# Optimization experiments

Measured on AMD Instinct MI355X. Metric: run time of the kernel, lower is better.

The kernel has to match this reference:

```python
import jax, jax.numpy as jnp
import numpy as np

INSTANCE_LOSS_WEIGHT = 5.0


def setup_inputs() -> dict:
    key = jax.random.key(0)
    k1, k2 = jax.random.split(key)
    B, NP, NT, H, W = 8, 8, 16, 512, 512
    pred_masks = jax.random.normal(k1, (B, NP, H, W), dtype=jnp.float32)   # logits
    target_masks = jax.random.uniform(k2, (B, NT, H, W), dtype=jnp.float32)  # targets in [0,1]
    return {"pred_masks": pred_masks, "target_masks": target_masks}


def reference(pred_masks, target_masks):
    # Multi-instance branch of SAMLossMultiInstance.forward (pred_masks.shape[1] > 1).
    # Original: per (i,j) pair, mean BCE-with-logits over pixels; pairs where
    # target j is all-zero are skipped (loss_matrix entry stays 0). Then
    # min over targets, mean over preds, mean over batch, * instance_loss_weight.
    #
    # Closed form: BCE(x, t) = softplus(x) - x*t, so
    #   mean_pix BCE(x_i, t_j) = mean(softplus(x_i)) - (x_i . t_j) / HW
    B, NP, H, W = pred_masks.shape
    HW = H * W
    s = jnp.mean(jax.nn.softplus(pred_masks), axis=(-2, -1))               # [B, NP]
    dots = jnp.einsum('bihw,bjhw->bij', pred_masks, target_masks) / HW     # [B, NP, NT]
    loss_matrix = s[:, :, None] - dots                                     # [B, NP, NT]
    # Empty targets are skipped in the original loop -> entry stays 0.
    t_empty = jnp.sum(target_masks, axis=(-2, -1)) == 0                    # [B, NT]
    loss_matrix = jnp.where(t_empty[:, None, :], 0.0, loss_matrix)
    min_losses = jnp.min(loss_matrix, axis=-1)                             # [B, NP]
    instance_loss = jnp.mean(min_losses)
    total_loss = INSTANCE_LOSS_WEIGHT * instance_loss
    return total_loss
```

## Files before the change

### kernel.cpp

```cpp
#include <hip/hip_runtime.h>

#define NB 8
#define NP 8
#define NT 16
#define HW (512 * 512)
#define HW4 (HW / 4)
#define NACC (NP + NP * NT + NT)
#define THREADS 256
#define BLOCKS_PER_B 256
#define NROW 32
#define LDSPITCH 153

__device__ __forceinline__ float softplus1(float x) {
  return fmaxf(x, 0.0f) + __logf(1.0f + __expf(-fabsf(x)));
}

__global__ __launch_bounds__(THREADS, 4) void sam_partial(
    const float* __restrict__ pred, const float* __restrict__ targ,
    float* __restrict__ ws) {
  const int b   = blockIdx.x >> 8;
  const int blk = blockIdx.x & 255;
  const int tid = threadIdx.x;
  const int idx = (blk << 8) | tid;
  const int lane = tid & 63;
  const int wid  = tid >> 6;
  const int row  = (wid << 3) | (lane >> 3);
  const bool wr  = (lane & 7) == 0;

  __shared__ float red[NROW][LDSPITCH];

  const float4* __restrict__ pb =
      reinterpret_cast<const float4*>(pred) + (size_t)b * NP * HW4;
  const float4* __restrict__ tb =
      reinterpret_cast<const float4*>(targ) + (size_t)b * NT * HW4;

  float4 p[NP];
#pragma unroll
  for (int i = 0; i < NP; ++i) p[i] = pb[(size_t)i * HW4 + idx];
  float4 t[NT];
#pragma unroll
  for (int j = 0; j < NT; ++j) t[j] = tb[(size_t)j * HW4 + idx];

#define STASH(a, expr)                                   \
  {                                                      \
    float v_ = (expr);                                   \
    v_ += __shfl_down(v_, 4);                            \
    v_ += __shfl_down(v_, 2);                            \
    v_ += __shfl_down(v_, 1);                            \
    if (wr) red[row][(a)] = v_;                          \
  }

#pragma unroll
  for (int i = 0; i < NP; ++i) {
    STASH(i, (softplus1(p[i].x) + softplus1(p[i].y)) +
             (softplus1(p[i].z) + softplus1(p[i].w)));
  }
#pragma unroll
  for (int i = 0; i < NP; ++i) {
#pragma unroll
    for (int j = 0; j < NT; ++j) {
      STASH(NP + i * NT + j,
            fmaf(p[i].x, t[j].x,
            fmaf(p[i].y, t[j].y,
            fmaf(p[i].z, t[j].z, p[i].w * t[j].w))));
    }
  }
#pragma unroll
  for (int j = 0; j < NT; ++j) {
    STASH(NP + NP * NT + j, (t[j].x + t[j].y) + (t[j].z + t[j].w));
  }
#undef STASH

  __syncthreads();
  if (tid < NACC) {
    float v = 0.0f;
#pragma unroll
    for (int r = 0; r < NROW; ++r) v += red[r][tid];
    atomicAdd(ws + (size_t)b * NACC + tid, v);
  }
}

__global__ void sam_final(const float* __restrict__ ws,
                          float* __restrict__ out) {
  const int t = threadIdx.x;
  const int b = t >> 3;
  const int i = t & 7;
  const float* w = ws + (size_t)b * NACC;
  const float spsum = w[i];
  float m = 3.4e38f;
#pragma unroll
  for (int j = 0; j < NT; ++j) {
    const float tsj = w[NP + NP * NT + j];
    const float v =
        (tsj == 0.0f) ? 0.0f : (spsum - w[NP + i * NT + j]) * (1.0f / HW);
    m = fminf(m, v);
  }
  float s = m;
#pragma unroll
  for (int off = 32; off > 0; off >>= 1) s += __shfl_down(s, off);
  if (t == 0) out[0] = 5.0f * s * (1.0f / 64.0f);
}

extern "C" void kernel_launch(void* const* d_in, const int* in_sizes, int n_in,
                              void* d_out, int out_size, void* d_ws,
                              size_t ws_size, hipStream_t stream) {
  const float* pred = (const float*)d_in[0];
  const float* targ = (const float*)d_in[1];
  float* out = (float*)d_out;
  float* ws = (float*)d_ws;

  hipMemsetAsync(ws, 0, (size_t)NB * NACC * sizeof(float), stream);
  sam_partial<<<dim3(NB * BLOCKS_PER_B), THREADS, 0, stream>>>(pred, targ, ws);
  sam_final<<<1, 64, 0, stream>>>(ws, out);
}
```

Baseline: 87.36 us.

## Split targets across waves and accumulate per-thread over pixel loop

Reassigns work so each wave owns two target masks and loops over several pixel chunks, accumulating dot products, target sums and one pred's softplus in registers. Per-element shuffle reductions into LDS and the block-wide LDS reduction are replaced by one wave reduction per accumulator at the end plus global atomics. This cuts reduction overhead and register pressure, allowing higher occupancy. The cost is that each pred element is reloaded by eight waves, relying on cache, and there are more global atomics.

```diff
diff --git a/kernel.cpp b/kernel.cpp
--- a/kernel.cpp
+++ b/kernel.cpp
@@ -7,76 +7,86 @@
 #define HW4 (HW / 4)
 #define NACC (NP + NP * NT + NT)
 #define THREADS 256
-#define BLOCKS_PER_B 256
-#define NROW 32
-#define LDSPITCH 153
+#define KITERS 8
 
 __device__ __forceinline__ float softplus1(float x) {
   return fmaxf(x, 0.0f) + __logf(1.0f + __expf(-fabsf(x)));
 }
 
-__global__ __launch_bounds__(THREADS, 4) void sam_partial(
+__device__ __forceinline__ float wred(float v) {
+#pragma unroll
+  for (int off = 32; off > 0; off >>= 1) v += __shfl_down(v, off);
+  return v;
+}
+
+__global__ __launch_bounds__(THREADS, 8) void sam_partial(
     const float* __restrict__ pred, const float* __restrict__ targ,
     float* __restrict__ ws) {
-  const int b   = blockIdx.x >> 8;
-  const int blk = blockIdx.x & 255;
-  const int tid = threadIdx.x;
-  const int idx = (blk << 8) | tid;
-  const int lane = tid & 63;
-  const int wid  = tid >> 6;
-  const int row  = (wid << 3) | (lane >> 3);
-  const bool wr  = (lane & 7) == 0;
-
-  __shared__ float red[NROW][LDSPITCH];
+  const int lane  = threadIdx.x & 63;
+  const int wid   = threadIdx.x >> 6;
+  const int half  = blockIdx.x & 1;
+  const int bs    = blockIdx.x >> 1;
+  const int b     = bs >> 7;
+  const int slice = bs & 127;
+  const int jp    = (half << 2) | wid;
 
   const float4* __restrict__ pb =
       reinterpret_cast<const float4*>(pred) + (size_t)b * NP * HW4;
-  const float4* __restrict__ tb =
-      reinterpret_cast<const float4*>(targ) + (size_t)b * NT * HW4;
+  const float4* __restrict__ t0b =
+      reinterpret_cast<const float4*>(targ) + (size_t)(b * NT + 2 * jp) * HW4;
+  const float4* __restrict__ t1b = t0b + HW4;
+  const float4* __restrict__ pj = pb + (size_t)jp * HW4;
 
-  float4 p[NP];
+  float dot[NP][2];
 #pragma unroll
-  for (int i = 0; i < NP; ++i) p[i] = pb[(size_t)i * HW4 + idx];
-  float4 t[NT];
+  for (int i = 0; i < NP; ++i) { dot[i][0] = 0.0f; dot[i][1] = 0.0f; }
+  float ts0 = 0.0f, ts1 = 0.0f, sp = 0.0f;
+
+  int idx = slice * (64 * KITERS) + lane;
+#pragma unroll 1
+  for (int k = 0; k < KITERS; ++k, idx += 64) {
+    const float4 t0 = t0b[idx];
+    const float4 t1 = t1b[idx];
+    ts0 += (t0.x + t0.y) + (t0.z + t0.w);
+    ts1 += (t1.x + t1.y) + (t1.z + t1.w);
 #pragma unroll
-  for (int j = 0; j < NT; ++j) t[j] = tb[(size_t)j * HW4 + idx];
-
-#define STASH(a, expr)                                   \
-  {                                                      \
-    float v_ = (expr);                                   \
-    v_ += __shfl_down(v_, 4);                            \
-    v_ += __shfl_down(v_, 2);                            \
-    v_ += __shfl_down(v_, 1);                            \
-    if (wr) red[row][(a)] = v_;                          \
+    for (int h = 0; h < 2; ++h) {
+      float4 p[4];
+#pragma unroll
+      for (int u = 0; u < 4; ++u) p[u] = pb[(size_t)(h * 4 + u) * HW4 + idx];
+#pragma unroll
+      for (int u = 0; u < 4; ++u) {
+        const int i = h * 4 + u;
+        dot[i][0] = fmaf(p[u].x, t0.x, fmaf(p[u].y, t0.y,
+                    fmaf(p[u].z, t0.z, fmaf(p[u].w, t0.w, dot[i][0]))));
+        dot[i][1] = fmaf(p[u].x, t1.x, fmaf(p[u].y, t1.y,
+                    fmaf(p[u].z, t1.z, fmaf(p[u].w, t1.w, dot[i][1]))));
+      }
+    }
+    const float4 q = pj[idx];
+    sp += (softplus1(q.x) + softplus1(q.y)) + (softplus1(q.z) + softplus1(q.w));
   }
 
-#pragma unroll
-  for (int i = 0; i < NP; ++i) {
-    STASH(i, (softplus1(p[i].x) + softplus1(p[i].y)) +
-             (softplus1(p[i].z) + softplus1(p[i].w)));
+  float* wb = ws + (size_t)b * NACC;
+  {
+    const float v = wred(sp);
+    if (lane == 0) atomicAdd(wb + jp, v);
   }
 #pragma unroll
   for (int i = 0; i < NP; ++i) {
 #pragma unroll
-    for (int j = 0; j < NT; ++j) {
-      STASH(NP + i * NT + j,
-            fmaf(p[i].x, t[j].x,
-            fmaf(p[i].y, t[j].y,
-            fmaf(p[i].z, t[j].z, p[i].w * t[j].w))));
+    for (int jj = 0; jj < 2; ++jj) {
+      const float v = wred(dot[i][jj]);
+      if (lane == 0) atomicAdd(wb + NP + i * NT + 2 * jp + jj, v);
     }
   }
-#pragma unroll
-  for (int j = 0; j < NT; ++j) {
-    STASH(NP + NP * NT + j, (t[j].x + t[j].y) + (t[j].z + t[j].w));
+  {
+    const float v = wred(ts0);
+    if (lane == 0) atomicAdd(wb + NP + NP * NT + 2 * jp, v);
   }
-#undef STASH
-
-  __syncthreads();
-  if (tid < NACC) {
-    float v = 0.0f;
-#pragma unroll
-    for (int r = 0; r < NROW; ++r) v += red[r][tid];
-    atomicAdd(ws + (size_t)b * NACC + tid, v);
+  {
+    const float v = wred(ts1);
+    if (lane == 0) atomicAdd(wb + NP + NP * NT + 2 * jp + 1, v);
   }
 }
 
@@ -110,6 +120,6 @@
   float* ws = (float*)d_ws;
 
   hipMemsetAsync(ws, 0, (size_t)NB * NACC * sizeof(float), stream);
-  sam_partial<<<dim3(NB * BLOCKS_PER_B), THREADS, 0, stream>>>(pred, targ, ws);
+  sam_partial<<<dim3(NB * 128 * 2), THREADS, 0, stream>>>(pred, targ, ws);
   sam_final<<<1, 64, 0, stream>>>(ws, out);
 }
```

Result: slower. 123.0 us (+40.8%).
